# Kernel tuning notes

Hardware: AMD Instinct MI355X
Metric: run time of the kernel (lower is better)

Reference implementation:

```python
import jax, jax.numpy as jnp
import numpy as np

EPS = 1e-5
NUM_HEADS = 16
NUM_KV_HEADS = 4
HEAD_DIM = 64
TOP_K = 2


def _layer_norm(x, w, b):
    m = jnp.mean(x, axis=-1, keepdims=True)
    v = jnp.mean((x - m) ** 2, axis=-1, keepdims=True)
    return (x - m) * jax.lax.rsqrt(v + EPS) * w + b


def setup_inputs() -> dict:
    key = jax.random.key(0)
    ks = jax.random.split(key, 8)
    S, B, H = 2048, 1, 1024
    E, F = 8, 4096
    q_per_kv = NUM_HEADS // NUM_KV_HEADS
    qkv_out = NUM_KV_HEADS * (q_per_kv + 2) * HEAD_DIM  # 1536

    def w(k, shape, scale=0.02):
        return jax.random.normal(k, shape, dtype=jnp.float32) * scale

    return {
        "hidden_states": jax.random.normal(ks[0], (S, B, H), dtype=jnp.float32),
        "ln1_weight": jnp.ones((H,), jnp.float32),
        "ln1_bias": jnp.zeros((H,), jnp.float32),
        "ln2_weight": jnp.ones((H,), jnp.float32),
        "ln2_bias": jnp.zeros((H,), jnp.float32),
        "qkv_weight": w(ks[1], (qkv_out, H)),
        "proj_weight": w(ks[2], (H, H)),
        "router_weight": w(ks[3], (H, E)),
        "moe_w1": w(ks[4], (E, H, F)),
        "moe_w2": w(ks[5], (E, F, H)),
    }


def reference(hidden_states, ln1_weight, ln1_bias, ln2_weight, ln2_bias,
              qkv_weight, proj_weight, router_weight, moe_w1, moe_w2):
    S, B, H = hidden_states.shape
    D = HEAD_DIM
    Hq, Hkv = NUM_HEADS, NUM_KV_HEADS
    g = Hq // Hkv                      # queries per kv head (GQA group)
    scale = 1.0 / np.sqrt(D)

    # ---- attention block ----
    ln1_out = _layer_norm(hidden_states, ln1_weight, ln1_bias)
    qkv = ln1_out @ qkv_weight.T                      # [S,B,Hkv*(g+2)*D]
    qkv = qkv.reshape(S, B, Hkv, (g + 2) * D)
    q = qkv[..., : g * D].reshape(S, B, Hq, D)        # [S,B,Hq,D]
    k = qkv[..., g * D : (g + 1) * D]                 # [S,B,Hkv,D]
    v = qkv[..., (g + 1) * D :]                       # [S,B,Hkv,D]

    # cp_size == 1 -> Ulysses all-to-alls are identity
    q_bf = q.transpose(1, 2, 0, 3).reshape(B, Hkv, g, S, D)  # [B,Hkv,g,S,D]
    k_bf = k.transpose(1, 2, 0, 3)                           # [B,Hkv,S,D]
    v_bf = v.transpose(1, 2, 0, 3)

    scores = jnp.einsum("bkgsd,bktd->bkgst", q_bf, k_bf) * scale
    causal = jnp.tril(jnp.ones((S, S), dtype=bool))
    scores = jnp.where(causal, scores, jnp.float32(-1e30))
    probs = jax.nn.softmax(scores, axis=-1)
    attn = jnp.einsum("bkgst,bktd->bkgsd", probs, v_bf)      # [B,Hkv,g,S,D]
    attn = attn.reshape(B, Hq, S, D).transpose(2, 0, 1, 3).reshape(S, B, Hq * D)

    proj_out = attn @ proj_weight.T
    hidden_after_attn = hidden_states + proj_out

    # ---- MoE block ----
    ln2_out = _layer_norm(hidden_after_attn, ln2_weight, ln2_bias)
    x = ln2_out.reshape(-1, H)                        # [T,H]
    T = x.shape[0]

    logits = x @ router_weight                        # [T,E] (fp32)
    rprobs = jax.nn.softmax(logits, axis=-1)
    top_p, top_i = jax.lax.top_k(rprobs, TOP_K)       # [T,k]
    top_p = top_p / jnp.sum(top_p, axis=-1, keepdims=True)

    # ep_size == 1: dispatch/sort/all-to-all are a pure permutation; compute
    # each expert densely over all tokens, then gather the routed outputs
    # (identical math to sort+grouped-GEMM+unsort).
    fc1 = jnp.einsum("th,ehf->etf", x, moe_w1)        # [E,T,F]
    act = jax.nn.gelu(fc1, approximate=False)
    y = jnp.einsum("etf,efh->eth", act, moe_w2)       # [E,T,H]

    tok = jnp.arange(T)[:, None]                      # [T,1]
    gathered = y[top_i, tok, :]                       # [T,k,H]
    moe_out = jnp.sum(gathered * top_p[..., None], axis=1)  # [T,H]

    return hidden_after_attn + moe_out.reshape(S, B, H)
```

## Files before the change

### kernel.cpp

```cpp
#include <hip/hip_runtime.h>
#include <cstdint>
#include <cstddef>

typedef unsigned short u16;
typedef __attribute__((ext_vector_type(8))) short bf16x8;
typedef __attribute__((ext_vector_type(4))) float f32x4;

#define MFMA16(a, b, c) __builtin_amdgcn_mfma_f32_16x16x32_bf16((a), (b), (c), 0, 0, 0)

__device__ __forceinline__ u16 f2bf(float f) {
  uint32_t u = __builtin_bit_cast(uint32_t, f);
  u += 0x7fffu + ((u >> 16) & 1u);
  return (u16)(u >> 16);
}
__device__ __forceinline__ float bf2f(u16 h) {
  uint32_t u = ((uint32_t)h) << 16;
  return __builtin_bit_cast(float, u);
}

__device__ __forceinline__ void gload_lds16(const void* g, void* l) {
  __builtin_amdgcn_global_load_lds(
      (const __attribute__((address_space(1))) uint32_t*)g,
      (__attribute__((address_space(3))) uint32_t*)l, 16, 0, 0);
}

template<bool WRITE_LO, bool WRITE_F32>
__launch_bounds__(256)
__global__ void ln_kernel(const float* __restrict__ in,
                          const float* __restrict__ w, const float* __restrict__ b,
                          u16* __restrict__ out_hi, u16* __restrict__ out_lo,
                          float* __restrict__ out_f32)
{
  int row = blockIdx.x;
  int tid = threadIdx.x;
  const float* x = in + (size_t)row * 1024;
  float4 v = *(const float4*)(x + tid * 4);
  float s  = v.x + v.y + v.z + v.w;
  float s2 = v.x*v.x + v.y*v.y + v.z*v.z + v.w*v.w;
  #pragma unroll
  for (int d = 1; d < 64; d <<= 1) { s += __shfl_xor(s, d); s2 += __shfl_xor(s2, d); }
  __shared__ float red[2][4];
  int wid = tid >> 6;
  if ((tid & 63) == 0) { red[0][wid] = s; red[1][wid] = s2; }
  __syncthreads();
  s  = red[0][0] + red[0][1] + red[0][2] + red[0][3];
  s2 = red[1][0] + red[1][1] + red[1][2] + red[1][3];
  float mean = s * (1.0f / 1024.0f);
  float var  = s2 * (1.0f / 1024.0f) - mean * mean;
  float rstd = rsqrtf(var + 1e-5f);
  float vv[4] = {v.x, v.y, v.z, v.w};
  #pragma unroll
  for (int j = 0; j < 4; ++j) {
    int c = tid * 4 + j;
    float y = (vv[j] - mean) * rstd * w[c] + b[c];
    size_t idx = (size_t)row * 1024 + c;
    u16 hb = f2bf(y);
    out_hi[idx] = hb;
    if (WRITE_LO)  out_lo[idx] = f2bf(y - bf2f(hb));
    if (WRITE_F32) out_f32[idx] = y;
  }
}

__global__ void convert_split_kernel(const float* __restrict__ in,
                                     u16* __restrict__ hi, u16* __restrict__ lo, int n4)
{
  int i = blockIdx.x * blockDim.x + threadIdx.x;
  if (i >= n4) return;
  float4 v = *(const float4*)(in + (size_t)i * 4);
  float a[4] = {v.x, v.y, v.z, v.w};
  u16 hh[4], ll[4];
  #pragma unroll
  for (int j = 0; j < 4; ++j) {
    hh[j] = f2bf(a[j]);
    ll[j] = f2bf(a[j] - bf2f(hh[j]));
  }
  uint2 hp, lp;
  hp.x = (uint32_t)hh[0] | ((uint32_t)hh[1] << 16);
  hp.y = (uint32_t)hh[2] | ((uint32_t)hh[3] << 16);
  lp.x = (uint32_t)ll[0] | ((uint32_t)ll[1] << 16);
  lp.y = (uint32_t)ll[2] | ((uint32_t)ll[3] << 16);
  *(uint2*)(hi + (size_t)i * 4) = hp;
  *(uint2*)(lo + (size_t)i * 4) = lp;
}

__global__ void transpose_convert_kernel(const float* __restrict__ in, u16* __restrict__ out,
                                         int R, int C)
{
  __shared__ float t[32][33];
  size_t ebase = (size_t)blockIdx.z * R * C;
  int c0 = blockIdx.x * 32, r0 = blockIdx.y * 32;
  int tx = threadIdx.x, ty = threadIdx.y;
  #pragma unroll
  for (int i = 0; i < 4; ++i)
    t[ty + 8*i][tx] = in[ebase + (size_t)(r0 + ty + 8*i) * C + (c0 + tx)];
  __syncthreads();
  #pragma unroll
  for (int i = 0; i < 4; ++i)
    out[ebase + (size_t)(c0 + ty + 8*i) * R + (r0 + tx)] = f2bf(t[tx][ty + 8*i]);
}

__global__ void vtrans_kernel(const u16* __restrict__ qkv, u16* __restrict__ vT)
{
  __shared__ u16 t[32][34];
  int kvh = blockIdx.z;
  int s0 = blockIdx.x * 32, d0 = blockIdx.y * 32;
  int tx = threadIdx.x, ty = threadIdx.y;
  #pragma unroll
  for (int i = 0; i < 4; ++i)
    t[ty + 8*i][tx] = qkv[(size_t)(s0 + ty + 8*i) * 1536 + kvh * 384 + 320 + d0 + tx];
  __syncthreads();
  #pragma unroll
  for (int i = 0; i < 4; ++i)
    vT[((size_t)kvh * 64 + d0 + ty + 8*i) * 2048 + (s0 + tx)] = t[tx][ty + 8*i];
}

template<int MODE>
__launch_bounds__(256, (MODE < 2) ? 2 : 4)
__global__ void gemm_kernel(const u16* __restrict__ Ahi, const u16* __restrict__ Alo,
                            const u16* __restrict__ Bhi, const u16* __restrict__ Blo,
                            int N, int K,
                            u16* __restrict__ Cb_hi, u16* __restrict__ Cb_lo,
                            float* __restrict__ Cf, const float* __restrict__ resid,
                            const int* __restrict__ tok_of_pair,
                            const int* __restrict__ counts, const int* __restrict__ prefix)
{
  constexpr bool SPLIT = (MODE < 2);
  int bn = blockIdx.x, bm = blockIdx.y;
  int row_base = 0;
  int count = 1 << 30;
  int kbeg = 0, kend = K;
  if constexpr (MODE >= 2) {
    int L = blockIdx.x + 32 * (blockIdx.y + 16 * blockIdx.z);
    int xcd = L & 7, idx = L >> 3;
    int e;
    if constexpr (MODE == 2) {
      bn = idx & 31;
      e  = xcd;
      bm = (idx >> 5) & 15;
    } else {
      bn = idx & 7;
      int G = xcd * 64 + (idx >> 3);
      int s = G >> 7;
      int rem = G & 127;
      e  = rem >> 4;
      bm = rem & 15;
      int kc = K >> 2;
      kbeg = s * kc; kend = kbeg + kc;
      Cb_hi += (size_t)s * 4096 * 1024;
    }
    count = counts[e];
    if (bm * 128 >= count) return;
    row_base = prefix[e];
    Bhi += (size_t)e * N * K;
  }
  __shared__ u16 As[2][SPLIT ? 2 : 1][128 * 32];
  __shared__ u16 Bs[2][SPLIT ? 2 : 1][128 * 32];

  int tid = threadIdx.x;
  int lane = tid & 63;
  int lo16 = lane & 15, hi4 = lane >> 4;
  int wid = tid >> 6, wr = wid >> 1, wc = wid & 1;

  const u16* gA[2][2];
  const u16* gB[2][2];
  int eidx[2];
  #pragma unroll
  for (int q = 0; q < 2; ++q) {
    int el = (q * 256 + tid) * 8;
    int r = el >> 5;
    int kc = ((((el >> 3) & 3) ^ ((r >> 1) & 3)) * 8);
    eidx[q] = el;
    if constexpr (MODE == 2) {
      int lim = count - bm * 128 - 1;
      int lr = r < lim ? r : lim;
      int token = tok_of_pair[row_base + bm * 128 + lr];
      gA[q][0] = Ahi + (size_t)token * K + kc;
    } else if constexpr (MODE == 3) {
      int lim = count - bm * 128 - 1;
      int lr = r < lim ? r : lim;
      gA[q][0] = Ahi + (size_t)(row_base + bm * 128 + lr) * K + kc;
    } else {
      gA[q][0] = Ahi + (size_t)(bm * 128 + r) * K + kc;
      gA[q][1] = Alo + (size_t)(bm * 128 + r) * K + kc;
    }
    gB[q][0] = Bhi + (size_t)(bn * 128 + r) * K + kc;
    if constexpr (SPLIT) gB[q][1] = Blo + (size_t)(bn * 128 + r) * K + kc;
  }

  auto stage = [&](int buf, int k0) {
    #pragma unroll
    for (int q = 0; q < 2; ++q) {
      gload_lds16(gA[q][0] + k0, &As[buf][0][eidx[q]]);
      gload_lds16(gB[q][0] + k0, &Bs[buf][0][eidx[q]]);
      if constexpr (SPLIT) {
        gload_lds16(gA[q][1] + k0, &As[buf][1][eidx[q]]);
        gload_lds16(gB[q][1] + k0, &Bs[buf][1][eidx[q]]);
      }
    }
  };

  const f32x4 zf = {0.f, 0.f, 0.f, 0.f};
  f32x4 acc[4][4];
  #pragma unroll
  for (int m = 0; m < 4; ++m)
    #pragma unroll
    for (int n = 0; n < 4; ++n) acc[m][n] = zf;

  stage(0, kbeg);
  __syncthreads();

  int csw = ((hi4 ^ ((lo16 >> 1) & 3)) * 8);

  int cur = 0;
  for (int k0 = kbeg; k0 < kend; k0 += 32, cur ^= 1) {
    if (k0 + 32 < kend) stage(cur ^ 1, k0 + 32);

    bf16x8 a0[4], b0[4], a1[4], b1[4];
    #pragma unroll
    for (int m = 0; m < 4; ++m)
      a0[m] = *(const bf16x8*)&As[cur][0][(wr * 64 + m * 16 + lo16) * 32 + csw];
    #pragma unroll
    for (int n = 0; n < 4; ++n)
      b0[n] = *(const bf16x8*)&Bs[cur][0][(wc * 64 + n * 16 + lo16) * 32 + csw];
    if constexpr (SPLIT) {
      #pragma unroll
      for (int m = 0; m < 4; ++m)
        a1[m] = *(const bf16x8*)&As[cur][1][(wr * 64 + m * 16 + lo16) * 32 + csw];
      #pragma unroll
      for (int n = 0; n < 4; ++n)
        b1[n] = *(const bf16x8*)&Bs[cur][1][(wc * 64 + n * 16 + lo16) * 32 + csw];
    }
    #pragma unroll
    for (int m = 0; m < 4; ++m)
      #pragma unroll
      for (int n = 0; n < 4; ++n) {
        acc[m][n] = MFMA16(a0[m], b0[n], acc[m][n]);
        if constexpr (SPLIT) {
          acc[m][n] = MFMA16(a0[m], b1[n], acc[m][n]);
          acc[m][n] = MFMA16(a1[m], b0[n], acc[m][n]);
        }
      }
    __syncthreads();
  }

  #pragma unroll
  for (int m = 0; m < 4; ++m)
    #pragma unroll
    for (int n = 0; n < 4; ++n)
      #pragma unroll
      for (int r = 0; r < 4; ++r) {
        int lr = wr * 64 + m * 16 + hi4 * 4 + r;
        int col = bn * 128 + wc * 64 + n * 16 + lo16;
        float v = acc[m][n][r];
        if constexpr (MODE == 0) {
          size_t idx = (size_t)(bm * 128 + lr) * N + col;
          u16 hb = f2bf(v);
          Cb_hi[idx] = hb;
          Cb_lo[idx] = f2bf(v - bf2f(hb));
        } else if constexpr (MODE == 1) {
          size_t idx = (size_t)(bm * 128 + lr) * N + col;
          Cf[idx] = v + resid[idx];
        } else if constexpr (MODE == 2) {
          if (bm * 128 + lr < count) {
            size_t idx = (size_t)(row_base + bm * 128 + lr) * N + col;
            float g = 0.5f * v * (1.0f + erff(v * 0.70710678118654752f));
            Cb_hi[idx] = f2bf(g);
          }
        } else {
          if (bm * 128 + lr < count) {
            size_t idx = (size_t)(row_base + bm * 128 + lr) * N + col;
            Cb_hi[idx] = f2bf(v);
          }
        }
      }
}

struct QState {
  bf16x8 qf[2][2];
  f32x4 o[4];
  float m_r[4], l_r[4];
  int qrow[4];
};

__device__ __forceinline__ void qstate_init(QState& S,
    const u16* qkv_hi, const u16* qkv_lo, int q0w, int qoff, int lo16, int hi4)
{
  const u16* ph = qkv_hi + (size_t)(q0w + lo16) * 1536 + qoff + hi4 * 8;
  const u16* pl = qkv_lo + (size_t)(q0w + lo16) * 1536 + qoff + hi4 * 8;
  S.qf[0][0] = *(const bf16x8*)ph;  S.qf[0][1] = *(const bf16x8*)(ph + 32);
  S.qf[1][0] = *(const bf16x8*)pl;  S.qf[1][1] = *(const bf16x8*)(pl + 32);
  const f32x4 zf = {0.f, 0.f, 0.f, 0.f};
  #pragma unroll
  for (int r = 0; r < 4; ++r) { S.m_r[r] = -INFINITY; S.l_r[r] = 0.f; S.qrow[r] = q0w + hi4 * 4 + r; }
  #pragma unroll
  for (int n = 0; n < 4; ++n) S.o[n] = zf;
}

__device__ __forceinline__ void attn_tile(QState& S, int kv0,
    const u16* Ks0, const u16* Ks1, const u16* Vs0, const u16* Vs1,
    u16* Ps0, u16* Ps1, int lo16, int hi4)
{
  const f32x4 zf = {0.f, 0.f, 0.f, 0.f};
  f32x4 sc[4];
  __builtin_amdgcn_s_setprio(1);
  #pragma unroll
  for (int c2 = 0; c2 < 4; ++c2) {
    sc[c2] = zf;
    int krow = c2 * 16 + lo16;
    const u16* kb  = &Ks0[krow * 64];
    const u16* kbl = &Ks1[krow * 64];
    bf16x8 kh0 = *(const bf16x8*)&kb [((hi4    ) ^ (krow & 7)) * 8];
    bf16x8 kh1 = *(const bf16x8*)&kb [((hi4 + 4) ^ (krow & 7)) * 8];
    bf16x8 kl0 = *(const bf16x8*)&kbl[((hi4    ) ^ (krow & 7)) * 8];
    bf16x8 kl1 = *(const bf16x8*)&kbl[((hi4 + 4) ^ (krow & 7)) * 8];
    sc[c2] = MFMA16(S.qf[0][0], kh0, sc[c2]);
    sc[c2] = MFMA16(S.qf[0][1], kh1, sc[c2]);
    sc[c2] = MFMA16(S.qf[0][0], kl0, sc[c2]);
    sc[c2] = MFMA16(S.qf[0][1], kl1, sc[c2]);
    sc[c2] = MFMA16(S.qf[1][0], kh0, sc[c2]);
    sc[c2] = MFMA16(S.qf[1][1], kh1, sc[c2]);
  }
  __builtin_amdgcn_s_setprio(0);

  float tmax[4] = {-INFINITY, -INFINITY, -INFINITY, -INFINITY};
  #pragma unroll
  for (int c2 = 0; c2 < 4; ++c2) {
    int kv = kv0 + c2 * 16 + lo16;
    #pragma unroll
    for (int r = 0; r < 4; ++r) {
      float sv = sc[c2][r] * 0.125f;
      if (kv > S.qrow[r]) sv = -1e30f;
      sc[c2][r] = sv;
      tmax[r] = fmaxf(tmax[r], sv);
    }
  }
  #pragma unroll
  for (int d = 1; d < 16; d <<= 1)
    #pragma unroll
    for (int r = 0; r < 4; ++r)
      tmax[r] = fmaxf(tmax[r], __shfl_xor(tmax[r], d));
  float rs[4], rowsum[4];
  #pragma unroll
  for (int r = 0; r < 4; ++r) {
    float mn = fmaxf(S.m_r[r], tmax[r]);
    rs[r] = __expf(S.m_r[r] - mn);
    S.m_r[r] = mn;
    rowsum[r] = 0.f;
  }
  #pragma unroll
  for (int c2 = 0; c2 < 4; ++c2)
    #pragma unroll
    for (int r = 0; r < 4; ++r) {
      float pv = __expf(sc[c2][r] - S.m_r[r]);
      sc[c2][r] = pv;
      rowsum[r] += pv;
    }
  #pragma unroll
  for (int d = 1; d < 16; d <<= 1)
    #pragma unroll
    for (int r = 0; r < 4; ++r)
      rowsum[r] += __shfl_xor(rowsum[r], d);
  #pragma unroll
  for (int r = 0; r < 4; ++r) S.l_r[r] = S.l_r[r] * rs[r] + rowsum[r];
  #pragma unroll
  for (int n = 0; n < 4; ++n)
    #pragma unroll
    for (int r = 0; r < 4; ++r) S.o[n][r] *= rs[r];

  #pragma unroll
  for (int c2 = 0; c2 < 4; ++c2)
    #pragma unroll
    for (int r = 0; r < 4; ++r) {
      float pv = sc[c2][r];
      u16 ph = f2bf(pv);
      int pidx = (hi4 * 4 + r) * 72 + c2 * 16 + lo16;
      Ps0[pidx] = ph;
      Ps1[pidx] = f2bf(pv - bf2f(ph));
    }

  __builtin_amdgcn_s_setprio(1);
  #pragma unroll
  for (int k2 = 0; k2 < 2; ++k2) {
    bf16x8 pah = *(const bf16x8*)&Ps0[lo16 * 72 + k2 * 32 + hi4 * 8];
    bf16x8 pal = *(const bf16x8*)&Ps1[lo16 * 72 + k2 * 32 + hi4 * 8];
    #pragma unroll
    for (int n = 0; n < 4; ++n) {
      int vrow = n * 16 + lo16;
      bf16x8 vh = *(const bf16x8*)&Vs0[vrow * 64 + (((k2 * 4 + hi4) ^ (vrow & 7))) * 8];
      bf16x8 vl = *(const bf16x8*)&Vs1[vrow * 64 + (((k2 * 4 + hi4) ^ (vrow & 7))) * 8];
      S.o[n] = MFMA16(pah, vh, S.o[n]);
      S.o[n] = MFMA16(pah, vl, S.o[n]);
      S.o[n] = MFMA16(pal, vh, S.o[n]);
    }
  }
  __builtin_amdgcn_s_setprio(0);
}

__device__ __forceinline__ void qstate_out(QState& S, int q0w, int h,
    u16* out_hi, u16* out_lo, int lo16, int hi4)
{
  #pragma unroll
  for (int n = 0; n < 4; ++n)
    #pragma unroll
    for (int r = 0; r < 4; ++r) {
      float v = S.o[n][r] / S.l_r[r];
      size_t idx = (size_t)(q0w + hi4 * 4 + r) * 1024 + h * 64 + n * 16 + lo16;
      u16 hb = f2bf(v);
      out_hi[idx] = hb;
      out_lo[idx] = f2bf(v - bf2f(hb));
    }
}

__launch_bounds__(256)
__global__ void attn_kernel(const u16* __restrict__ qkv_hi, const u16* __restrict__ qkv_lo,
                            const u16* __restrict__ vT_hi, const u16* __restrict__ vT_lo,
                            u16* __restrict__ out_hi, u16* __restrict__ out_lo)
{
  int id = blockIdx.y * 32 + blockIdx.x;
  int h = id & 15;
  int j = (id >> 4) & 15;
  int qb = (id < 256) ? (31 - j) : j;
  int kvh = h >> 2, gi = h & 3;
  int tid = threadIdx.x;
  int lane = tid & 63;
  int w = tid >> 6;
  int lo16 = lane & 15, hi4 = lane >> 4;
  int q0w = qb * 64 + w * 16;
  int qoff = kvh * 384 + gi * 64;
  int koff = kvh * 384 + 256;

  __shared__ u16 Ks[2][64 * 64];
  __shared__ u16 Vs[2][64 * 64];
  __shared__ u16 Ps[2][4][16 * 72];
  u16* Ps0 = &Ps[0][w][0];
  u16* Ps1 = &Ps[1][w][0];

  QState S;
  qstate_init(S, qkv_hi, qkv_lo, q0w, qoff, lo16, hi4);

  for (int t = 0; t <= qb; ++t) {
    int kv0 = t * 64;
    __syncthreads();
    #pragma unroll
    for (int it = 0; it < 2; ++it) {
      int u = it * 256 + tid;
      int row = u >> 3, ch = u & 7;
      int d = (ch ^ (row & 7)) * 8;
      *(uint4*)&Ks[0][row * 64 + d] = *(const uint4*)(qkv_hi + (size_t)(kv0 + row) * 1536 + koff + ch * 8);
      *(uint4*)&Ks[1][row * 64 + d] = *(const uint4*)(qkv_lo + (size_t)(kv0 + row) * 1536 + koff + ch * 8);
      *(uint4*)&Vs[0][row * 64 + d] = *(const uint4*)(vT_hi + ((size_t)kvh * 64 + row) * 2048 + kv0 + ch * 8);
      *(uint4*)&Vs[1][row * 64 + d] = *(const uint4*)(vT_lo + ((size_t)kvh * 64 + row) * 2048 + kv0 + ch * 8);
    }
    __syncthreads();

    attn_tile(S, kv0, Ks[0], Ks[1], Vs[0], Vs[1], Ps0, Ps1, lo16, hi4);
  }

  qstate_out(S, q0w, h, out_hi, out_lo, lo16, hi4);
}

__launch_bounds__(64)
__global__ void router_kernel(const float* __restrict__ x, const float* __restrict__ rw,
                              int* __restrict__ counts, int* __restrict__ esel,
                              int* __restrict__ slotsel, float* __restrict__ wsel)
{
  int t = blockIdx.x;
  int l = threadIdx.x;
  float acc[8] = {0.f, 0.f, 0.f, 0.f, 0.f, 0.f, 0.f, 0.f};
  const float* xr = x + (size_t)t * 1024;
  for (int hh = l; hh < 1024; hh += 64) {
    float xv = xr[hh];
    const float* wp = rw + hh * 8;
    #pragma unroll
    for (int e = 0; e < 8; ++e) acc[e] = fmaf(xv, wp[e], acc[e]);
  }
  #pragma unroll
  for (int e = 0; e < 8; ++e)
    #pragma unroll
    for (int d = 1; d < 64; d <<= 1) acc[e] += __shfl_xor(acc[e], d);
  if (l == 0) {
    int e1 = 0;
    #pragma unroll
    for (int e = 1; e < 8; ++e) if (acc[e] > acc[e1]) e1 = e;
    int e2 = -1;
    #pragma unroll
    for (int e = 0; e < 8; ++e) {
      if (e == e1) continue;
      if (e2 < 0 || acc[e] > acc[e2]) e2 = e;
    }
    float p1 = 1.0f / (1.0f + expf(acc[e2] - acc[e1]));
    float p2 = 1.0f - p1;
    int s1 = atomicAdd(&counts[e1], 1);
    int s2 = atomicAdd(&counts[e2], 1);
    esel[t * 2] = e1; esel[t * 2 + 1] = e2;
    slotsel[t * 2] = s1; slotsel[t * 2 + 1] = s2;
    wsel[t * 2] = p1; wsel[t * 2 + 1] = p2;
  }
}

__global__ void build_lists_kernel(const int* __restrict__ counts, int* __restrict__ prefix,
                                   const int* __restrict__ esel, const int* __restrict__ slotsel,
                                   int* __restrict__ tok_of_pair, int* __restrict__ pair_idx)
{
  __shared__ int pfx[8];
  if (threadIdx.x == 0) {
    int a = 0;
    for (int e = 0; e < 8; ++e) { pfx[e] = a; prefix[e] = a; a += counts[e]; }
  }
  __syncthreads();
  for (int t = threadIdx.x; t < 2048; t += 256) {
    #pragma unroll
    for (int k = 0; k < 2; ++k) {
      int e = esel[t * 2 + k];
      int row = pfx[e] + slotsel[t * 2 + k];
      tok_of_pair[row] = t;
      pair_idx[t * 2 + k] = row;
    }
  }
}

__launch_bounds__(256)
__global__ void final_kernel(const float* __restrict__ hattn, const u16* __restrict__ y,
                             const int* __restrict__ pair_idx, const float* __restrict__ wsel,
                             float* __restrict__ out)
{
  int t = blockIdx.x;
  int c = threadIdx.x * 4;
  int p0 = pair_idx[t * 2], p1 = pair_idx[t * 2 + 1];
  float w0 = wsel[t * 2], w1 = wsel[t * 2 + 1];
  float4 a = *(const float4*)(hattn + (size_t)t * 1024 + c);
  float y0[4] = {0.f, 0.f, 0.f, 0.f};
  float y1[4] = {0.f, 0.f, 0.f, 0.f};
  #pragma unroll
  for (int s = 0; s < 4; ++s) {
    const u16* base = y + (size_t)s * 4096 * 1024;
    uint2 v0 = *(const uint2*)(base + (size_t)p0 * 1024 + c);
    uint2 v1 = *(const uint2*)(base + (size_t)p1 * 1024 + c);
    y0[0] += bf2f((u16)(v0.x & 0xffff)); y0[1] += bf2f((u16)(v0.x >> 16));
    y0[2] += bf2f((u16)(v0.y & 0xffff)); y0[3] += bf2f((u16)(v0.y >> 16));
    y1[0] += bf2f((u16)(v1.x & 0xffff)); y1[1] += bf2f((u16)(v1.x >> 16));
    y1[2] += bf2f((u16)(v1.y & 0xffff)); y1[3] += bf2f((u16)(v1.y >> 16));
  }
  float4 r;
  r.x = a.x + w0 * y0[0] + w1 * y1[0];
  r.y = a.y + w0 * y0[1] + w1 * y1[1];
  r.z = a.z + w0 * y0[2] + w1 * y1[2];
  r.w = a.w + w0 * y0[3] + w1 * y1[3];
  *(float4*)(out + (size_t)t * 1024 + c) = r;
}

extern "C" void kernel_launch(void* const* d_in, const int* in_sizes, int n_in,
                              void* d_out, int out_size, void* d_ws, size_t ws_size,
                              hipStream_t stream)
{
  const float* hidden   = (const float*)d_in[0];
  const float* ln1_w    = (const float*)d_in[1];
  const float* ln1_b    = (const float*)d_in[2];
  const float* ln2_w    = (const float*)d_in[3];
  const float* ln2_b    = (const float*)d_in[4];
  const float* qkv_w    = (const float*)d_in[5];
  const float* proj_w   = (const float*)d_in[6];
  const float* router_w = (const float*)d_in[7];
  const float* moe_w1   = (const float*)d_in[8];
  const float* moe_w2   = (const float*)d_in[9];
  float* out = (float*)d_out;

  char* ws = (char*)d_ws;
  size_t off = 0;
  auto alloc = [&](size_t bytes) -> void* {
    void* p = (void*)(ws + off);
    off += (bytes + 255) & ~(size_t)255;
    return p;
  };

  u16* wT      = (u16*)alloc(8ull * 4096 * 1024 * 2);
  float* hattn = (float*)alloc(2048ull * 1024 * 4);
  u16* x_hi    = (u16*)alloc(2048ull * 1024 * 2);
  u16* act     = (u16*)alloc(4096ull * 4096 * 2);
  u16* ybuf    = (u16*)alloc(4ull * 4096 * 1024 * 4);

  char* ov = (char*)ybuf;
  size_t oo = 0;
  auto oalloc = [&](size_t bytes) -> void* {
    void* p = (void*)(ov + oo);
    oo += (bytes + 255) & ~(size_t)255;
    return p;
  };
  u16* ln1_hi  = (u16*)oalloc(2048ull * 1024 * 2);
  u16* ln1_lo  = (u16*)oalloc(2048ull * 1024 * 2);
  u16* qw_hi   = (u16*)oalloc(1536ull * 1024 * 2);
  u16* qw_lo   = (u16*)oalloc(1536ull * 1024 * 2);
  u16* pw_hi   = (u16*)oalloc(1024ull * 1024 * 2);
  u16* pw_lo   = (u16*)oalloc(1024ull * 1024 * 2);
  u16* qkv_hi  = (u16*)oalloc(2048ull * 1536 * 2);
  u16* qkv_lo  = (u16*)oalloc(2048ull * 1536 * 2);
  u16* vt_hi   = (u16*)oalloc(4ull * 64 * 2048 * 2);
  u16* vt_lo   = (u16*)oalloc(4ull * 64 * 2048 * 2);
  u16* at_hi   = (u16*)oalloc(2048ull * 1024 * 2);
  u16* at_lo   = (u16*)oalloc(2048ull * 1024 * 2);
  float* x_f32 = (float*)oalloc(2048ull * 1024 * 4);

  int* counts  = (int*)alloc(8 * 4);
  int* prefix  = (int*)alloc(8 * 4);
  int* esel    = (int*)alloc(2048ull * 2 * 4);
  int* slotsel = (int*)alloc(2048ull * 2 * 4);
  int* topair  = (int*)alloc(4096ull * 4);
  int* pairidx = (int*)alloc(2048ull * 2 * 4);
  float* wsel  = (float*)alloc(2048ull * 2 * 4);

  hipMemsetAsync(counts, 0, 8 * 4, stream);

  ln_kernel<true, false><<<2048, 256, 0, stream>>>(hidden, ln1_w, ln1_b, ln1_hi, ln1_lo, nullptr);

  convert_split_kernel<<<1536, 256, 0, stream>>>(qkv_w, qw_hi, qw_lo, 1536 * 1024 / 4);
  convert_split_kernel<<<1024, 256, 0, stream>>>(proj_w, pw_hi, pw_lo, 1024 * 1024 / 4);

  gemm_kernel<0><<<dim3(12, 16, 1), 256, 0, stream>>>(
      ln1_hi, ln1_lo, qw_hi, qw_lo, 1536, 1024,
      qkv_hi, qkv_lo, nullptr, nullptr, nullptr, nullptr, nullptr);

  vtrans_kernel<<<dim3(64, 2, 4), dim3(32, 8), 0, stream>>>(qkv_hi, vt_hi);
  vtrans_kernel<<<dim3(64, 2, 4), dim3(32, 8), 0, stream>>>(qkv_lo, vt_lo);

  attn_kernel<<<dim3(32, 16), 256, 0, stream>>>(qkv_hi, qkv_lo, vt_hi, vt_lo, at_hi, at_lo);

  gemm_kernel<1><<<dim3(8, 16, 1), 256, 0, stream>>>(
      at_hi, at_lo, pw_hi, pw_lo, 1024, 1024,
      nullptr, nullptr, hattn, hidden, nullptr, nullptr, nullptr);

  ln_kernel<false, true><<<2048, 256, 0, stream>>>(hattn, ln2_w, ln2_b, x_hi, nullptr, x_f32);

  router_kernel<<<2048, 64, 0, stream>>>(x_f32, router_w, counts, esel, slotsel, wsel);
  build_lists_kernel<<<1, 256, 0, stream>>>(counts, prefix, esel, slotsel, topair, pairidx);

  transpose_convert_kernel<<<dim3(128, 32, 8), dim3(32, 8), 0, stream>>>(moe_w1, wT, 1024, 4096);

  gemm_kernel<2><<<dim3(32, 16, 8), 256, 0, stream>>>(
      x_hi, nullptr, wT, nullptr, 4096, 1024,
      act, nullptr, nullptr, nullptr, topair, counts, prefix);

  transpose_convert_kernel<<<dim3(32, 128, 8), dim3(32, 8), 0, stream>>>(moe_w2, wT, 4096, 1024);

  gemm_kernel<3><<<dim3(32, 16, 8), 256, 0, stream>>>(
      act, nullptr, wT, nullptr, 1024, 4096,
      ybuf, nullptr, nullptr, nullptr, topair, counts, prefix);

  final_kernel<<<2048, 256, 0, stream>>>(hattn, ybuf, pairidx, wsel, out);
}
```

Baseline: 467.5 us.

## Triple-buffer LDS and use one barrier per iteration in MoE expert GEMMs

For the non-split expert GEMM modes, the shared-memory staging grows from two to three buffers. Loads for tile t+2 are issued while tile t is computed, and manual vmcnt waits replace the full syncthreads, leaving a single barrier per k-step. The aim is to hide global load latency better and cut synchronisation stalls. In exchange, LDS use rises, so the occupancy hint drops from 4 to 3 blocks per CU.

```diff
diff --git a/kernel.cpp b/kernel.cpp
--- a/kernel.cpp
+++ b/kernel.cpp
@@ -115,7 +115,7 @@
 }
 
 template<int MODE>
-__launch_bounds__(256, (MODE < 2) ? 2 : 4)
+__launch_bounds__(256, (MODE < 2) ? 2 : 3)
 __global__ void gemm_kernel(const u16* __restrict__ Ahi, const u16* __restrict__ Alo,
                             const u16* __restrict__ Bhi, const u16* __restrict__ Blo,
                             int N, int K,
@@ -153,8 +153,8 @@
     row_base = prefix[e];
     Bhi += (size_t)e * N * K;
   }
-  __shared__ u16 As[2][SPLIT ? 2 : 1][128 * 32];
-  __shared__ u16 Bs[2][SPLIT ? 2 : 1][128 * 32];
+  __shared__ u16 As[SPLIT ? 2 : 3][SPLIT ? 2 : 1][128 * 32];
+  __shared__ u16 Bs[SPLIT ? 2 : 3][SPLIT ? 2 : 1][128 * 32];
 
   int tid = threadIdx.x;
   int lane = tid & 63;
@@ -206,41 +206,74 @@
     #pragma unroll
     for (int n = 0; n < 4; ++n) acc[m][n] = zf;
 
-  stage(0, kbeg);
-  __syncthreads();
-
   int csw = ((hi4 ^ ((lo16 >> 1) & 3)) * 8);
 
-  int cur = 0;
-  for (int k0 = kbeg; k0 < kend; k0 += 32, cur ^= 1) {
-    if (k0 + 32 < kend) stage(cur ^ 1, k0 + 32);
-
-    bf16x8 a0[4], b0[4], a1[4], b1[4];
-    #pragma unroll
-    for (int m = 0; m < 4; ++m)
-      a0[m] = *(const bf16x8*)&As[cur][0][(wr * 64 + m * 16 + lo16) * 32 + csw];
-    #pragma unroll
-    for (int n = 0; n < 4; ++n)
-      b0[n] = *(const bf16x8*)&Bs[cur][0][(wc * 64 + n * 16 + lo16) * 32 + csw];
-    if constexpr (SPLIT) {
+  if constexpr (!SPLIT) {
+    const int nt = (kend - kbeg) >> 5;
+    stage(0, kbeg);
+    if (nt > 1) {
+      stage(1, kbeg + 32);
+      asm volatile("s_waitcnt vmcnt(4)" ::: "memory");
+    } else {
+      asm volatile("s_waitcnt vmcnt(0)" ::: "memory");
+    }
+    __builtin_amdgcn_s_barrier();
+
+    int rb = 0, sb = 2;
+    for (int t = 0; t < nt; ++t) {
+      if (t + 2 < nt) stage(sb, kbeg + (t + 2) * 32);
+
+      bf16x8 a0[4], b0[4];
+      #pragma unroll
+      for (int m = 0; m < 4; ++m)
+        a0[m] = *(const bf16x8*)&As[rb][0][(wr * 64 + m * 16 + lo16) * 32 + csw];
+      #pragma unroll
+      for (int n = 0; n < 4; ++n)
+        b0[n] = *(const bf16x8*)&Bs[rb][0][(wc * 64 + n * 16 + lo16) * 32 + csw];
+      #pragma unroll
+      for (int m = 0; m < 4; ++m)
+        #pragma unroll
+        for (int n = 0; n < 4; ++n)
+          acc[m][n] = MFMA16(a0[m], b0[n], acc[m][n]);
+
+      if (t + 1 < nt) {
+        if (t + 2 < nt) asm volatile("s_waitcnt vmcnt(4)" ::: "memory");
+        else            asm volatile("s_waitcnt vmcnt(0)" ::: "memory");
+        __builtin_amdgcn_s_barrier();
+      }
+      rb = (rb == 2) ? 0 : rb + 1;
+      sb = (sb == 2) ? 0 : sb + 1;
+    }
+  } else {
+    stage(0, kbeg);
+    __syncthreads();
+    int cur = 0;
+    for (int k0 = kbeg; k0 < kend; k0 += 32, cur ^= 1) {
+      if (k0 + 32 < kend) stage(cur ^ 1, k0 + 32);
+
+      bf16x8 a0[4], b0[4], a1[4], b1[4];
+      #pragma unroll
+      for (int m = 0; m < 4; ++m)
+        a0[m] = *(const bf16x8*)&As[cur][0][(wr * 64 + m * 16 + lo16) * 32 + csw];
+      #pragma unroll
+      for (int n = 0; n < 4; ++n)
+        b0[n] = *(const bf16x8*)&Bs[cur][0][(wc * 64 + n * 16 + lo16) * 32 + csw];
       #pragma unroll
       for (int m = 0; m < 4; ++m)
         a1[m] = *(const bf16x8*)&As[cur][1][(wr * 64 + m * 16 + lo16) * 32 + csw];
       #pragma unroll
       for (int n = 0; n < 4; ++n)
         b1[n] = *(const bf16x8*)&Bs[cur][1][(wc * 64 + n * 16 + lo16) * 32 + csw];
-    }
-    #pragma unroll
-    for (int m = 0; m < 4; ++m)
-      #pragma unroll
-      for (int n = 0; n < 4; ++n) {
-        acc[m][n] = MFMA16(a0[m], b0[n], acc[m][n]);
-        if constexpr (SPLIT) {
+      #pragma unroll
+      for (int m = 0; m < 4; ++m)
+        #pragma unroll
+        for (int n = 0; n < 4; ++n) {
+          acc[m][n] = MFMA16(a0[m], b0[n], acc[m][n]);
           acc[m][n] = MFMA16(a0[m], b1[n], acc[m][n]);
           acc[m][n] = MFMA16(a1[m], b0[n], acc[m][n]);
         }
-      }
-    __syncthreads();
+      __syncthreads();
+    }
   }
 
   #pragma unroll
```

After: 462.1 us. About the same (-1.2%).

## Split long causal attention query blocks across two KV halves with combine kernel

Applied to the files above, without the earlier changes.

Query blocks 16-31 are split into two workgroups, each processing half of the KV tiles and writing unnormalized partial outputs plus row max and sum to scratch. A new combine kernel merges the two partials with log-sum-exp rescaling and writes the split bf16 hi/lo output. Short query blocks still run unsplit. This evens out per-workgroup work across 768 blocks to cut the causal tail imbalance, at the cost of an extra launch and fp32 scratch traffic.

```diff
diff --git a/kernel.cpp b/kernel.cpp
--- a/kernel.cpp
+++ b/kernel.cpp
@@ -414,12 +414,27 @@
 __launch_bounds__(256)
 __global__ void attn_kernel(const u16* __restrict__ qkv_hi, const u16* __restrict__ qkv_lo,
                             const u16* __restrict__ vT_hi, const u16* __restrict__ vT_lo,
-                            u16* __restrict__ out_hi, u16* __restrict__ out_lo)
-{
-  int id = blockIdx.y * 32 + blockIdx.x;
-  int h = id & 15;
-  int j = (id >> 4) & 15;
-  int qb = (id < 256) ? (31 - j) : j;
+                            u16* __restrict__ out_hi, u16* __restrict__ out_lo,
+                            float* __restrict__ part_o, float* __restrict__ part_ml)
+{
+  int id = blockIdx.x;
+  int h, qb, t0, t1, part = 0;
+  bool split;
+  if (id < 512) {
+    qb = 31 - (id >> 5);
+    h = (id >> 1) & 15;
+    part = id & 1;
+    int nh = (qb + 1) >> 1;
+    t0 = part ? nh : 0;
+    t1 = part ? (qb + 1) : nh;
+    split = true;
+  } else {
+    int rr = id - 512;
+    qb = 15 - (rr >> 4);
+    h = rr & 15;
+    t0 = 0; t1 = qb + 1;
+    split = false;
+  }
   int kvh = h >> 2, gi = h & 3;
   int tid = threadIdx.x;
   int lane = tid & 63;
@@ -438,7 +453,7 @@
   QState S;
   qstate_init(S, qkv_hi, qkv_lo, q0w, qoff, lo16, hi4);
 
-  for (int t = 0; t <= qb; ++t) {
+  for (int t = t0; t < t1; ++t) {
     int kv0 = t * 64;
     __syncthreads();
     #pragma unroll
@@ -456,7 +471,53 @@
     attn_tile(S, kv0, Ks[0], Ks[1], Vs[0], Vs[1], Ps0, Ps1, lo16, hi4);
   }
 
-  qstate_out(S, q0w, h, out_hi, out_lo, lo16, hi4);
+  if (!split) {
+    qstate_out(S, q0w, h, out_hi, out_lo, lo16, hi4);
+  } else {
+    int pj = ((qb - 16) * 16 + h) * 2 + part;
+    float* po  = part_o  + (size_t)pj * 4096;
+    float* pml = part_ml + (size_t)pj * 128;
+    #pragma unroll
+    for (int n = 0; n < 4; ++n)
+      #pragma unroll
+      for (int r = 0; r < 4; ++r)
+        po[(w * 16 + hi4 * 4 + r) * 64 + n * 16 + lo16] = S.o[n][r];
+    if (lo16 == 0) {
+      #pragma unroll
+      for (int r = 0; r < 4; ++r) {
+        pml[w * 16 + hi4 * 4 + r] = S.m_r[r];
+        pml[64 + w * 16 + hi4 * 4 + r] = S.l_r[r];
+      }
+    }
+  }
+}
+
+__launch_bounds__(256)
+__global__ void attn_combine(const float* __restrict__ part_o, const float* __restrict__ part_ml,
+                             u16* __restrict__ out_hi, u16* __restrict__ out_lo)
+{
+  int job = blockIdx.x;
+  int qb = 16 + (job >> 4);
+  int h = job & 15;
+  const float* po0  = part_o  + (size_t)(job * 2    ) * 4096;
+  const float* po1  = part_o  + (size_t)(job * 2 + 1) * 4096;
+  const float* pml0 = part_ml + (size_t)(job * 2    ) * 128;
+  const float* pml1 = part_ml + (size_t)(job * 2 + 1) * 128;
+  int t = threadIdx.x;
+  #pragma unroll
+  for (int i = 0; i < 16; ++i) {
+    int e = i * 256 + t;
+    int row = e >> 6, col = e & 63;
+    float m0 = pml0[row], m1 = pml1[row];
+    float M = fmaxf(m0, m1);
+    float e0 = __expf(m0 - M), e1 = __expf(m1 - M);
+    float l = pml0[64 + row] * e0 + pml1[64 + row] * e1;
+    float v = (po0[row * 64 + col] * e0 + po1[row * 64 + col] * e1) / l;
+    size_t idx = (size_t)(qb * 64 + row) * 1024 + h * 64 + col;
+    u16 hb = f2bf(v);
+    out_hi[idx] = hb;
+    out_lo[idx] = f2bf(v - bf2f(hb));
+  }
 }
 
 __launch_bounds__(64)
@@ -599,6 +660,8 @@
   u16* at_hi   = (u16*)oalloc(2048ull * 1024 * 2);
   u16* at_lo   = (u16*)oalloc(2048ull * 1024 * 2);
   float* x_f32 = (float*)oalloc(2048ull * 1024 * 4);
+  float* part_o  = (float*)oalloc(512ull * 4096 * 4);
+  float* part_ml = (float*)oalloc(512ull * 128 * 4);
 
   int* counts  = (int*)alloc(8 * 4);
   int* prefix  = (int*)alloc(8 * 4);
@@ -622,7 +685,8 @@
   vtrans_kernel<<<dim3(64, 2, 4), dim3(32, 8), 0, stream>>>(qkv_hi, vt_hi);
   vtrans_kernel<<<dim3(64, 2, 4), dim3(32, 8), 0, stream>>>(qkv_lo, vt_lo);
 
-  attn_kernel<<<dim3(32, 16), 256, 0, stream>>>(qkv_hi, qkv_lo, vt_hi, vt_lo, at_hi, at_lo);
+  attn_kernel<<<768, 256, 0, stream>>>(qkv_hi, qkv_lo, vt_hi, vt_lo, at_hi, at_lo, part_o, part_ml);
+  attn_combine<<<256, 256, 0, stream>>>(part_o, part_ml, at_hi, at_lo);
 
   gemm_kernel<1><<<dim3(8, 16, 1), 256, 0, stream>>>(
       at_hi, at_lo, pw_hi, pw_lo, 1024, 1024,
```

Measured after the change: 460.1 us. No clear change (-1.6%).
